# Optimization experiments

Measured on AMD Instinct MI355X. Metric: run time of the kernel, lower is better.

The kernel has to match this reference:

```python
import jax, jax.numpy as jnp
import numpy as np

N = 20000
E = 320000
IN_DIM, HID, OUT_DIM = 32, 64, 4
HEADS = 4
NEG_SLOPE = 0.2


def _self_loops(src, dst):
    loop = jnp.arange(N, dtype=src.dtype)
    return jnp.concatenate([src, loop]), jnp.concatenate([dst, loop])


def gcn_conv(x, W, b, src, dst):
    h = x @ W                                            # [N, C]
    es, ed = _self_loops(src, dst)
    deg = jax.ops.segment_sum(jnp.ones_like(es, dtype=h.dtype), ed, num_segments=N)
    dinv = jnp.where(deg > 0, jax.lax.rsqrt(deg), 0.0)
    norm = dinv[es] * dinv[ed]                           # [E']
    out = jax.ops.segment_sum(h[es] * norm[:, None], ed, num_segments=N)
    return out + b


def gat_conv(x, W, att_src, att_dst, b, src, dst):
    # PyG GATConv: heads concat, self-loops, leaky_relu(0.2), softmax over incoming edges per dst
    H, C = att_src.shape
    h = (x @ W).reshape(N, H, C)                         # [N, H, C]
    a_s = jnp.sum(h * att_src, axis=-1)                  # [N, H]
    a_d = jnp.sum(h * att_dst, axis=-1)                  # [N, H]
    es, ed = _self_loops(src, dst)
    logits = jax.nn.leaky_relu(a_s[es] + a_d[ed], NEG_SLOPE)   # [E', H]
    m = jax.ops.segment_max(logits, ed, num_segments=N)
    expv = jnp.exp(logits - m[ed])
    denom = jax.ops.segment_sum(expv, ed, num_segments=N)
    alpha = expv / denom[ed]                             # [E', H]
    out = jax.ops.segment_sum(h[es] * alpha[:, :, None], ed, num_segments=N)
    return out.reshape(N, H * C) + b


def setup_inputs() -> dict:
    key = jax.random.key(0)
    ks = iter(jax.random.split(key, 32))
    s = 0.05
    def w(shape):
        return jax.random.normal(next(ks), shape, dtype=jnp.float32) * s
    inp = {}
    inp["x"] = jax.random.normal(next(ks), (N, IN_DIM), dtype=jnp.float32)
    inp["edge_index"] = jax.random.randint(next(ks), (2, E), 0, N, dtype=jnp.int32)
    # encoder1 GCN 32->64; encoder2 GCN 64->128; encoder3 GAT 128->128 x4 heads
    inp["w_e1"], inp["b_e1"] = w((IN_DIM, HID)), jnp.zeros((HID,), jnp.float32)
    inp["w_e2"], inp["b_e2"] = w((HID, 2 * HID)), jnp.zeros((2 * HID,), jnp.float32)
    inp["w_e3"] = w((2 * HID, HEADS * 2 * HID))
    inp["as_e3"], inp["ad_e3"] = w((HEADS, 2 * HID)), w((HEADS, 2 * HID))
    inp["b_e3"] = jnp.zeros((HEADS * 2 * HID,), jnp.float32)
    # decoder1 GCN 1024->128; decoder2 GCN 128->64; decoder3 GAT 64->64 x4 heads
    inp["w_d1"], inp["b_d1"] = w((HEADS * 2 * HID, 2 * HID)), jnp.zeros((2 * HID,), jnp.float32)
    inp["w_d2"], inp["b_d2"] = w((2 * HID, HID)), jnp.zeros((HID,), jnp.float32)
    inp["w_d3"] = w((HID, HEADS * HID))
    inp["as_d3"], inp["ad_d3"] = w((HEADS, HID)), w((HEADS, HID))
    inp["b_d3"] = jnp.zeros((HEADS * HID,), jnp.float32)
    # MLP head 256->256->128->4
    inp["w_fc1"], inp["b_fc1"] = w((4 * HID, 4 * HID)), jnp.zeros((4 * HID,), jnp.float32)
    inp["w_fc2"], inp["b_fc2"] = w((4 * HID, 2 * HID)), jnp.zeros((2 * HID,), jnp.float32)
    inp["w_fin"], inp["b_fin"] = w((2 * HID, OUT_DIM)), jnp.zeros((OUT_DIM,), jnp.float32)
    return inp


def reference(x, edge_index, w_e1, b_e1, w_e2, b_e2, w_e3, as_e3, ad_e3, b_e3,
              w_d1, b_d1, w_d2, b_d2, w_d3, as_d3, ad_d3, b_d3,
              w_fc1, b_fc1, w_fc2, b_fc2, w_fin, b_fin):
    src, dst = edge_index[0], edge_index[1]
    relu = jax.nn.relu
    x1 = relu(gcn_conv(x, w_e1, b_e1, src, dst))
    x2 = relu(gcn_conv(x1, w_e2, b_e2, src, dst))
    x3 = relu(gat_conv(x2, w_e3, as_e3, ad_e3, b_e3, src, dst))
    h = relu(gcn_conv(x3, w_d1, b_d1, src, dst)) + x2
    h = relu(gcn_conv(h, w_d2, b_d2, src, dst)) + x1
    h = relu(gat_conv(h, w_d3, as_d3, ad_d3, b_d3, src, dst))
    h = relu(h @ w_fc1 + b_fc1)
    h = relu(h @ w_fc2 + b_fc2)
    return h @ w_fin + b_fin
```

## Files before the change

kernel.cpp:

```cpp
#include <hip/hip_runtime.h>
#include <cstdint>
#include <cstddef>

static constexpr int Nn = 20000;
static constexpr int Ee = 320000;

typedef _Float16 half8 __attribute__((ext_vector_type(8)));
typedef float f32x4 __attribute__((ext_vector_type(4)));

__device__ __forceinline__ float lrelu02(float x){ return fmaxf(x, 0.2f*x); }
__device__ __forceinline__ float af(int x){ return __int_as_float(x); }

__device__ __forceinline__ void packhl(float v, unsigned short& h, unsigned short& l){
  _Float16 hh = (_Float16)v;
  _Float16 ll = (_Float16)((v - (float)hh) * 2048.0f);
  h = __builtin_bit_cast(unsigned short, hh);
  l = __builtin_bit_cast(unsigned short, ll);
}

__global__ void k_scan(const int* __restrict__ cnt, int* __restrict__ row_start,
                       float* __restrict__ dinv){
  __shared__ int part[1024];
  int tid = threadIdx.x;
  const int PER = 20;
  int base = tid*PER;
  int s = 0;
  for (int i = 0; i < PER; ++i){ int idx = base+i; if (idx < Nn) s += cnt[idx]; }
  part[tid] = s; __syncthreads();
  for (int off = 1; off < 1024; off <<= 1){
    int v = (tid >= off) ? part[tid-off] : 0;
    __syncthreads();
    part[tid] += v;
    __syncthreads();
  }
  int run = (tid == 0) ? 0 : part[tid-1];
  for (int i = 0; i < PER; ++i){
    int idx = base+i;
    if (idx < Nn){
      row_start[idx] = run;
      int c = cnt[idx];
      run += c;
      dinv[idx] = rsqrtf((float)(c+1));
    }
  }
  if (tid == 1023) row_start[Nn] = run;
}

__global__ void k_scatter(const int* __restrict__ src, const int* __restrict__ dst,
                          const int* __restrict__ row_start, int* __restrict__ fill,
                          int* __restrict__ csr, const float* __restrict__ dinv,
                          int2* __restrict__ erec){
  int e = blockIdx.x*256 + threadIdx.x;
  if (e < Ee){
    int d = dst[e];
    int pos = row_start[d] + atomicAdd(&fill[d], 1);
    int u = src[e];
    csr[pos] = u;
    erec[pos] = make_int2(u, __float_as_int(dinv[u]));
  }
}

struct PrepArgs {
  const float *w_e1,*w_e2,*w_e3,*w_d1,*w_d2,*w_d3,*w_fc1,*w_fc2;
  unsigned short *p_e1,*p_e2,*p_e3,*p_d1,*p_d2,*p_d3,*p_fc1,*p_fc2;
  const float *as_e3,*ad_e3,*as_d3,*ad_d3;
  float *wsF_e3,*wdF_e3,*wsF_d3,*wdF_d3;
  const int* dst;
  int* cnt;
};

__device__ __forceinline__ void packw_one(const float* __restrict__ W,
                                          unsigned short* __restrict__ out,
                                          int i, int jlog, int K){
  int k = i >> jlog, col = i - (k << jlog);
  unsigned short h, l; packhl(W[i], h, l);
  size_t pos = ((size_t)((col>>4)*(K>>3) + (k>>3))*16 + (col&15))*8 + (k&7);
  out[pos] = h;
  out[pos + ((size_t)K << jlog)] = l;
}

__global__ void k_init(PrepArgs a){
  int gi = blockIdx.x*256 + threadIdx.x;
  if (gi >= 264960){
    int e = gi - 264960;
    if (e < Ee) atomicAdd(&a.cnt[a.dst[e]], 1);
    return;
  }
  int i = gi;
  if      (i <   2048) packw_one(a.w_e1,  a.p_e1,  i,          6,  32);
  else if (i <  10240) packw_one(a.w_e2,  a.p_e2,  i-2048,     7,  64);
  else if (i <  75776) packw_one(a.w_e3,  a.p_e3,  i-10240,    9, 128);
  else if (i < 141312) packw_one(a.w_d1,  a.p_d1,  i-75776,    7, 512);
  else if (i < 149504) packw_one(a.w_d2,  a.p_d2,  i-141312,   6, 128);
  else if (i < 165888) packw_one(a.w_d3,  a.p_d3,  i-149504,   8,  64);
  else if (i < 231424) packw_one(a.w_fc1, a.p_fc1, i-165888,   8, 256);
  else if (i < 264192) packw_one(a.w_fc2, a.p_fc2, i-231424,   7, 256);
  else if (i < 264704){
    int t = i - 264192;
    int h = t >> 7, k = t & 127;
    float s = 0.f, d = 0.f;
    #pragma unroll 4
    for (int c = 0; c < 128; ++c){
      float wv = a.w_e3[(size_t)k*512 + h*128 + c];
      s = fmaf(wv, a.as_e3[h*128 + c], s);
      d = fmaf(wv, a.ad_e3[h*128 + c], d);
    }
    a.wsF_e3[h*128 + k] = s;
    a.wdF_e3[h*128 + k] = d;
  } else {
    int t = i - 264704;
    int h = t >> 6, k = t & 63;
    float s = 0.f, d = 0.f;
    #pragma unroll 4
    for (int c = 0; c < 64; ++c){
      float wv = a.w_d3[(size_t)k*256 + h*64 + c];
      s = fmaf(wv, a.as_d3[h*64 + c], s);
      d = fmaf(wv, a.ad_d3[h*64 + c], d);
    }
    a.wsF_d3[h*64 + k] = s;
    a.wdF_d3[h*64 + k] = d;
  }
}

template<int C, int POST>
__global__ __launch_bounds__(256) void k_gcn_agg(
    const float* __restrict__ h, const float* __restrict__ dinv,
    const int* __restrict__ row_start, const int2* __restrict__ erec,
    const float* __restrict__ bias, const float* __restrict__ skip,
    float* __restrict__ outf, unsigned short* __restrict__ outp){
  int v = blockIdx.x*4 + (threadIdx.x >> 6);
  int lane = threadIdx.x & 63;
  int s = __builtin_amdgcn_readfirstlane(row_start[v]);
  int e = __builtin_amdgcn_readfirstlane(row_start[v+1]);
  float dv = dinv[v];
  const int c = (C==32) ? (lane & 31) : ((C==128) ? lane*2 : lane);

  float a0 = 0.f, a1 = 0.f;
  if constexpr (C == 32){
    int half = lane >> 5;
    int j = s + half;
    for (; j + 2 < e; j += 4){
      int2 r0 = erec[j], r1 = erec[j+2];
      float t0 = h[(size_t)r0.x*32 + c];
      float t1 = h[(size_t)r1.x*32 + c];
      a0 = fmaf(af(r0.y), t0, a0);
      a0 = fmaf(af(r1.y), t1, a0);
    }
    if (j < e){
      int2 r0 = erec[j];
      a0 = fmaf(af(r0.y), h[(size_t)r0.x*32 + c], a0);
    }
    a0 += __shfl_xor(a0, 32);
  } else if constexpr (C == 128){
    int j = s;
    for (; j + 4 <= e; j += 4){
      int2 r0 = erec[j], r1 = erec[j+1], r2 = erec[j+2], r3 = erec[j+3];
      float2 t0 = *(const float2*)&h[(size_t)r0.x*128 + c];
      float2 t1 = *(const float2*)&h[(size_t)r1.x*128 + c];
      float2 t2 = *(const float2*)&h[(size_t)r2.x*128 + c];
      float2 t3 = *(const float2*)&h[(size_t)r3.x*128 + c];
      a0=fmaf(af(r0.y),t0.x,a0); a1=fmaf(af(r0.y),t0.y,a1);
      a0=fmaf(af(r1.y),t1.x,a0); a1=fmaf(af(r1.y),t1.y,a1);
      a0=fmaf(af(r2.y),t2.x,a0); a1=fmaf(af(r2.y),t2.y,a1);
      a0=fmaf(af(r3.y),t3.x,a0); a1=fmaf(af(r3.y),t3.y,a1);
    }
    for (; j < e; ++j){
      int2 r = erec[j];
      float2 t = *(const float2*)&h[(size_t)r.x*128 + c];
      a0 = fmaf(af(r.y), t.x, a0); a1 = fmaf(af(r.y), t.y, a1);
    }
  } else {
    int j = s;
    for (; j + 4 <= e; j += 4){
      int2 r0 = erec[j], r1 = erec[j+1], r2 = erec[j+2], r3 = erec[j+3];
      float t0 = h[(size_t)r0.x*64 + c];
      float t1 = h[(size_t)r1.x*64 + c];
      float t2 = h[(size_t)r2.x*64 + c];
      float t3 = h[(size_t)r3.x*64 + c];
      a0=fmaf(af(r0.y),t0,a0); a0=fmaf(af(r1.y),t1,a0);
      a0=fmaf(af(r2.y),t2,a0); a0=fmaf(af(r3.y),t3,a0);
    }
    for (; j < e; ++j){
      int2 r = erec[j];
      a0 = fmaf(af(r.y), h[(size_t)r.x*64 + c], a0);
    }
  }

  if constexpr (C == 128){
    float2 hv = *(const float2*)&h[(size_t)v*128 + c];
    float vx = fmaf(a0, dv, hv.x*dv*dv);
    float vy = fmaf(a1, dv, hv.y*dv*dv);
    if constexpr (POST & 1){
      float2 bv = *(const float2*)&bias[c];
      float2 sk = *(const float2*)&skip[(size_t)v*128 + c];
      vx = fmaxf(vx + bv.x, 0.f) + sk.x;
      vy = fmaxf(vy + bv.y, 0.f) + sk.y;
    }
    if constexpr (POST & 2){
      unsigned short h0,l0,h1,l1; packhl(vx,h0,l0); packhl(vy,h1,l1);
      *(unsigned int*)&outp[(size_t)v*128 + c] = (unsigned)h0 | ((unsigned)h1<<16);
      *(unsigned int*)&outp[(size_t)v*128 + c + (size_t)Nn*128] = (unsigned)l0 | ((unsigned)l1<<16);
    } else {
      *(float2*)&outf[(size_t)v*128 + c] = make_float2(vx, vy);
    }
  } else if constexpr (C == 64){
    float val = fmaf(a0, dv, h[(size_t)v*64 + c]*dv*dv);
    if constexpr (POST & 1){
      val = fmaxf(val + bias[c], 0.f) + skip[(size_t)v*64 + c];
    }
    if constexpr (POST & 2){
      unsigned short hh,ll; packhl(val,hh,ll);
      outp[(size_t)v*64 + c] = hh;
      outp[(size_t)v*64 + c + (size_t)Nn*64] = ll;
    } else {
      outf[(size_t)v*64 + c] = val;
    }
  } else {
    float val = fmaf(a0, dv, h[(size_t)v*32 + c]*dv*dv);
    if (lane < 32){
      unsigned short hh,ll; packhl(val,hh,ll);
      outp[(size_t)v*32 + c] = hh;
      outp[(size_t)v*32 + c + (size_t)Nn*32] = ll;
    }
  }
}

template<int INC>
__global__ __launch_bounds__(256) void k_attn_in(
    const float* __restrict__ X, const float* __restrict__ wsF, const float* __restrict__ wdF,
    float* __restrict__ aS, float* __restrict__ aD){
  int v = blockIdx.x*4 + (threadIdx.x >> 6);
  int lane = threadIdx.x & 63;
  float x0 = X[(size_t)v*INC + lane];
  float x1 = (INC == 128) ? X[(size_t)v*INC + 64 + lane] : 0.f;
  float s[4], d[4];
  #pragma unroll
  for (int h = 0; h < 4; ++h){
    s[h] = x0*wsF[h*INC + lane];
    d[h] = x0*wdF[h*INC + lane];
    if constexpr (INC == 128){
      s[h] = fmaf(x1, wsF[h*INC + 64 + lane], s[h]);
      d[h] = fmaf(x1, wdF[h*INC + 64 + lane], d[h]);
    }
  }
  #pragma unroll
  for (int off = 32; off; off >>= 1){
    #pragma unroll
    for (int h = 0; h < 4; ++h){
      s[h] += __shfl_xor(s[h], off);
      d[h] += __shfl_xor(d[h], off);
    }
  }
  if (lane == 0){
    *(float4*)&aS[v*4] = make_float4(s[0], s[1], s[2], s[3]);
    *(float4*)&aD[v*4] = make_float4(d[0], d[1], d[2], d[3]);
  }
}

template<int INC>
__global__ __launch_bounds__(256) void k_gat_fused(
    const float* __restrict__ X, const int* __restrict__ csr,
    const float* __restrict__ aS, const float* __restrict__ aD,
    const int* __restrict__ row_start, unsigned short* __restrict__ outp){
  __shared__ float4 sF[4][64];
  int wv = threadIdx.x >> 6;
  int v = blockIdx.x*4 + wv;
  int lane = threadIdx.x & 63;
  int s = __builtin_amdgcn_readfirstlane(row_start[v]);
  int e = __builtin_amdgcn_readfirstlane(row_start[v+1]);
  const int c2 = lane*2;

  float4 tD = *(const float4*)&aD[v*4];
  float ad0=tD.x, ad1=tD.y, ad2=tD.z, ad3=tD.w;
  float4 tS = *(const float4*)&aS[v*4];

  float sd0=0.f, sd1=0.f, sd2=0.f, sd3=0.f;
  float2 acc0={0,0}, acc1={0,0}, acc2={0,0}, acc3={0,0};
  float ac0=0.f, ac1=0.f, ac2=0.f, ac3=0.f;

  for (int base = s; base < e; base += 64){
    int i = base + lane;
    float4 f = {0.f, 0.f, 0.f, 0.f};
    if (i < e){
      int u = csr[i];
      float4 a4 = *(const float4*)&aS[u*4];
      f.x = __expf(lrelu02(a4.x+ad0));
      f.y = __expf(lrelu02(a4.y+ad1));
      f.z = __expf(lrelu02(a4.z+ad2));
      f.w = __expf(lrelu02(a4.w+ad3));
      sd0 += f.x; sd1 += f.y; sd2 += f.z; sd3 += f.w;
    }
    sF[wv][lane] = f;
    int cnt = min(64, e - base);
    int j = 0;
    for (; j + 4 <= cnt; j += 4){
      int u0=csr[base+j], u1=csr[base+j+1], u2=csr[base+j+2], u3=csr[base+j+3];
      float4 f0=sF[wv][j], f1=sF[wv][j+1], f2=sF[wv][j+2], f3=sF[wv][j+3];
      if constexpr (INC == 128){
        float2 x0 = *(const float2*)&X[(size_t)u0*128 + c2];
        float2 x1 = *(const float2*)&X[(size_t)u1*128 + c2];
        float2 x2 = *(const float2*)&X[(size_t)u2*128 + c2];
        float2 x3 = *(const float2*)&X[(size_t)u3*128 + c2];
        acc0.x=fmaf(f0.x,x0.x,acc0.x); acc0.y=fmaf(f0.x,x0.y,acc0.y);
        acc1.x=fmaf(f0.y,x0.x,acc1.x); acc1.y=fmaf(f0.y,x0.y,acc1.y);
        acc2.x=fmaf(f0.z,x0.x,acc2.x); acc2.y=fmaf(f0.z,x0.y,acc2.y);
        acc3.x=fmaf(f0.w,x0.x,acc3.x); acc3.y=fmaf(f0.w,x0.y,acc3.y);
        acc0.x=fmaf(f1.x,x1.x,acc0.x); acc0.y=fmaf(f1.x,x1.y,acc0.y);
        acc1.x=fmaf(f1.y,x1.x,acc1.x); acc1.y=fmaf(f1.y,x1.y,acc1.y);
        acc2.x=fmaf(f1.z,x1.x,acc2.x); acc2.y=fmaf(f1.z,x1.y,acc2.y);
        acc3.x=fmaf(f1.w,x1.x,acc3.x); acc3.y=fmaf(f1.w,x1.y,acc3.y);
        acc0.x=fmaf(f2.x,x2.x,acc0.x); acc0.y=fmaf(f2.x,x2.y,acc0.y);
        acc1.x=fmaf(f2.y,x2.x,acc1.x); acc1.y=fmaf(f2.y,x2.y,acc1.y);
        acc2.x=fmaf(f2.z,x2.x,acc2.x); acc2.y=fmaf(f2.z,x2.y,acc2.y);
        acc3.x=fmaf(f2.w,x2.x,acc3.x); acc3.y=fmaf(f2.w,x2.y,acc3.y);
        acc0.x=fmaf(f3.x,x3.x,acc0.x); acc0.y=fmaf(f3.x,x3.y,acc0.y);
        acc1.x=fmaf(f3.y,x3.x,acc1.x); acc1.y=fmaf(f3.y,x3.y,acc1.y);
        acc2.x=fmaf(f3.z,x3.x,acc2.x); acc2.y=fmaf(f3.z,x3.y,acc2.y);
        acc3.x=fmaf(f3.w,x3.x,acc3.x); acc3.y=fmaf(f3.w,x3.y,acc3.y);
      } else {
        float x0 = X[(size_t)u0*64 + lane];
        float x1 = X[(size_t)u1*64 + lane];
        float x2 = X[(size_t)u2*64 + lane];
        float x3 = X[(size_t)u3*64 + lane];
        ac0=fmaf(f0.x,x0,ac0); ac1=fmaf(f0.y,x0,ac1); ac2=fmaf(f0.z,x0,ac2); ac3=fmaf(f0.w,x0,ac3);
        ac0=fmaf(f1.x,x1,ac0); ac1=fmaf(f1.y,x1,ac1); ac2=fmaf(f1.z,x1,ac2); ac3=fmaf(f1.w,x1,ac3);
        ac0=fmaf(f2.x,x2,ac0); ac1=fmaf(f2.y,x2,ac1); ac2=fmaf(f2.z,x2,ac2); ac3=fmaf(f2.w,x2,ac3);
        ac0=fmaf(f3.x,x3,ac0); ac1=fmaf(f3.y,x3,ac1); ac2=fmaf(f3.z,x3,ac2); ac3=fmaf(f3.w,x3,ac3);
      }
    }
    for (; j < cnt; ++j){
      int u = csr[base+j];
      float4 f4 = sF[wv][j];
      if constexpr (INC == 128){
        float2 xu = *(const float2*)&X[(size_t)u*128 + c2];
        acc0.x=fmaf(f4.x,xu.x,acc0.x); acc0.y=fmaf(f4.x,xu.y,acc0.y);
        acc1.x=fmaf(f4.y,xu.x,acc1.x); acc1.y=fmaf(f4.y,xu.y,acc1.y);
        acc2.x=fmaf(f4.z,xu.x,acc2.x); acc2.y=fmaf(f4.z,xu.y,acc2.y);
        acc3.x=fmaf(f4.w,xu.x,acc3.x); acc3.y=fmaf(f4.w,xu.y,acc3.y);
      } else {
        float xu = X[(size_t)u*64 + lane];
        ac0=fmaf(f4.x,xu,ac0); ac1=fmaf(f4.y,xu,ac1); ac2=fmaf(f4.z,xu,ac2); ac3=fmaf(f4.w,xu,ac3);
      }
    }
  }

  #pragma unroll
  for (int off = 32; off; off >>= 1){
    sd0 += __shfl_xor(sd0, off);
    sd1 += __shfl_xor(sd1, off);
    sd2 += __shfl_xor(sd2, off);
    sd3 += __shfl_xor(sd3, off);
  }
  float es0=__expf(lrelu02(tS.x+ad0)), es1=__expf(lrelu02(tS.y+ad1));
  float es2=__expf(lrelu02(tS.z+ad2)), es3=__expf(lrelu02(tS.w+ad3));
  float r0=1.f/(sd0+es0), r1=1.f/(sd1+es1), r2=1.f/(sd2+es2), r3=1.f/(sd3+es3);

  if constexpr (INC == 128){
    float2 xv = *(const float2*)&X[(size_t)v*128 + c2];
    const size_t loOff = (size_t)Nn*512;
    float ox, oy; unsigned short h0,l0,h1,l1;
    ox=(acc0.x+es0*xv.x)*r0; oy=(acc0.y+es0*xv.y)*r0;
    packhl(ox,h0,l0); packhl(oy,h1,l1);
    *(unsigned int*)&outp[(size_t)v*512 +   0 + c2] = (unsigned)h0|((unsigned)h1<<16);
    *(unsigned int*)&outp[(size_t)v*512 +   0 + c2 + loOff] = (unsigned)l0|((unsigned)l1<<16);
    ox=(acc1.x+es1*xv.x)*r1; oy=(acc1.y+es1*xv.y)*r1;
    packhl(ox,h0,l0); packhl(oy,h1,l1);
    *(unsigned int*)&outp[(size_t)v*512 + 128 + c2] = (unsigned)h0|((unsigned)h1<<16);
    *(unsigned int*)&outp[(size_t)v*512 + 128 + c2 + loOff] = (unsigned)l0|((unsigned)l1<<16);
    ox=(acc2.x+es2*xv.x)*r2; oy=(acc2.y+es2*xv.y)*r2;
    packhl(ox,h0,l0); packhl(oy,h1,l1);
    *(unsigned int*)&outp[(size_t)v*512 + 256 + c2] = (unsigned)h0|((unsigned)h1<<16);
    *(unsigned int*)&outp[(size_t)v*512 + 256 + c2 + loOff] = (unsigned)l0|((unsigned)l1<<16);
    ox=(acc3.x+es3*xv.x)*r3; oy=(acc3.y+es3*xv.y)*r3;
    packhl(ox,h0,l0); packhl(oy,h1,l1);
    *(unsigned int*)&outp[(size_t)v*512 + 384 + c2] = (unsigned)h0|((unsigned)h1<<16);
    *(unsigned int*)&outp[(size_t)v*512 + 384 + c2 + loOff] = (unsigned)l0|((unsigned)l1<<16);
  } else {
    float xv = X[(size_t)v*64 + lane];
    const size_t loOff = (size_t)Nn*256;
    unsigned short hh,ll;
    float o;
    o = (ac0+es0*xv)*r0; packhl(o,hh,ll);
    outp[(size_t)v*256 +   0 + lane] = hh; outp[(size_t)v*256 +   0 + lane + loOff] = ll;
    o = (ac1+es1*xv)*r1; packhl(o,hh,ll);
    outp[(size_t)v*256 +  64 + lane] = hh; outp[(size_t)v*256 +  64 + lane + loOff] = ll;
    o = (ac2+es2*xv)*r2; packhl(o,hh,ll);
    outp[(size_t)v*256 + 128 + lane] = hh; outp[(size_t)v*256 + 128 + lane + loOff] = ll;
    o = (ac3+es3*xv)*r3; packhl(o,hh,ll);
    outp[(size_t)v*256 + 192 + lane] = hh; outp[(size_t)v*256 + 192 + lane + loOff] = ll;
  }
}

template<int K, int J, int Jh, int EPI>
__global__ __launch_bounds__(256) void k_gemm(
    const unsigned short* __restrict__ Ahi, int lda,
    const unsigned short* __restrict__ Wp,
    const float* __restrict__ bias,
    float* __restrict__ outf, unsigned short* __restrict__ outp){
  __shared__ unsigned short sAhi[4*64*8], sAlo[4*64*8];
  __shared__ unsigned short sBhi[4*64*8], sBlo[4*64*8];

  const int tid  = threadIdx.x;
  const int lane = tid & 63, w = tid >> 6;
  const int rb = blockIdx.x;
  const int colbase = blockIdx.z*Jh + blockIdx.y*64;
  const int akoff   = blockIdx.z*K;
  const size_t AloOff = (size_t)Nn*lda;
  const size_t WloOff = (size_t)K*J;

  f32x4 accH[4] = {{0,0,0,0},{0,0,0,0},{0,0,0,0},{0,0,0,0}};
  f32x4 accM[4] = {{0,0,0,0},{0,0,0,0},{0,0,0,0},{0,0,0,0}};

  const int arow = tid >> 2;
  const int akq  = (tid & 3) * 8;
  int agrow = rb*64 + arow; if (agrow >= Nn) agrow = Nn - 1;
  const unsigned short* Ag = Ahi + (size_t)agrow*lda + akoff + akq;
  const int aw_idx = (((arow>>4)*4 + (akq>>3))*16 + (arow&15))*8;
  const int bcol = tid & 63;
  const int bkg  = tid >> 6;
  const int bw_idx = (((bcol>>4)*4 + bkg)*16 + (bcol&15))*8;
  const int cf_g  = (colbase>>4) + (bcol>>4);
  const size_t wbase = ((size_t)cf_g*(K/8)*16 + (size_t)(bcol&15))*8;

  #pragma unroll 1
  for (int ks = 0; ks < K/32; ++ks){
    if (ks) __syncthreads();
    {
      const unsigned short* p = Ag + ks*32;
      uint4 hv = *(const uint4*)p;
      uint4 lv = *(const uint4*)(p + AloOff);
      *(uint4*)&sAhi[aw_idx] = hv;
      *(uint4*)&sAlo[aw_idx] = lv;
    }
    {
      size_t goff = wbase + (size_t)(ks*4 + bkg)*128;
      uint4 hv = *(const uint4*)&Wp[goff];
      uint4 lv = *(const uint4*)&Wp[goff + WloOff];
      *(uint4*)&sBhi[bw_idx] = hv;
      *(uint4*)&sBlo[bw_idx] = lv;
    }
    __syncthreads();

    half8 aH = *(const half8*)&sAhi[(w*64 + lane)*8];
    half8 aL = *(const half8*)&sAlo[(w*64 + lane)*8];
    #pragma unroll
    for (int cf = 0; cf < 4; ++cf){
      half8 bH = *(const half8*)&sBhi[(cf*64 + lane)*8];
      half8 bL = *(const half8*)&sBlo[(cf*64 + lane)*8];
      accH[cf] = __builtin_amdgcn_mfma_f32_16x16x32_f16(aH, bH, accH[cf], 0, 0, 0);
      accM[cf] = __builtin_amdgcn_mfma_f32_16x16x32_f16(aH, bL, accM[cf], 0, 0, 0);
      accM[cf] = __builtin_amdgcn_mfma_f32_16x16x32_f16(aL, bH, accM[cf], 0, 0, 0);
    }
  }

  #pragma unroll
  for (int cf = 0; cf < 4; ++cf){
    int col = colbase + cf*16 + (lane & 15);
    float bv = (EPI >= 1) ? bias[col] : 0.f;
    #pragma unroll
    for (int r = 0; r < 4; ++r){
      int row = rb*64 + w*16 + ((lane>>4)*4 + r);
      if (row < Nn){
        float v = accH[cf][r] + accM[cf][r]*(1.0f/2048.0f);
        if constexpr (EPI >= 1) v = fmaxf(v + bv, 0.f);
        if constexpr (EPI == 2){
          unsigned short hh, ll; packhl(v, hh, ll);
          outp[(size_t)row*J + col] = hh;
          outp[(size_t)row*J + col + (size_t)Nn*J] = ll;
        } else {
          outf[(size_t)row*J + col] = v;
        }
      }
    }
  }
}

__global__ __launch_bounds__(256) void k_mm_fin(
    const float* __restrict__ A, const float* __restrict__ W,
    const float* __restrict__ bias, float* __restrict__ out){
  int row = blockIdx.x*4 + (threadIdx.x >> 6);
  int lane = threadIdx.x & 63;
  float a0 = A[(size_t)row*128 + lane];
  float a1 = A[(size_t)row*128 + 64 + lane];
  float4 w0 = ((const float4*)W)[lane];
  float4 w1 = ((const float4*)W)[64 + lane];
  float p0 = fmaf(a1, w1.x, a0*w0.x);
  float p1 = fmaf(a1, w1.y, a0*w0.y);
  float p2 = fmaf(a1, w1.z, a0*w0.z);
  float p3 = fmaf(a1, w1.w, a0*w0.w);
  #pragma unroll
  for (int off = 32; off; off >>= 1){
    p0 += __shfl_xor(p0, off);
    p1 += __shfl_xor(p1, off);
    p2 += __shfl_xor(p2, off);
    p3 += __shfl_xor(p3, off);
  }
  if (lane == 0){
    float4 bv = *(const float4*)bias;
    *(float4*)&out[(size_t)row*4] = make_float4(p0+bv.x, p1+bv.y, p2+bv.z, p3+bv.w);
  }
}

extern "C" void kernel_launch(void* const* d_in, const int* in_sizes, int n_in,
                              void* d_out, int out_size, void* d_ws, size_t ws_size,
                              hipStream_t stream){
  const float* x     = (const float*)d_in[0];
  const int*   ei    = (const int*)  d_in[1];
  const float* w_e1  = (const float*)d_in[2];
  const float* b_e1  = (const float*)d_in[3];
  const float* w_e2  = (const float*)d_in[4];
  const float* b_e2  = (const float*)d_in[5];
  const float* w_e3  = (const float*)d_in[6];
  const float* as_e3 = (const float*)d_in[7];
  const float* ad_e3 = (const float*)d_in[8];
  const float* b_e3  = (const float*)d_in[9];
  const float* w_d1  = (const float*)d_in[10];
  const float* b_d1  = (const float*)d_in[11];
  const float* w_d2  = (const float*)d_in[12];
  const float* b_d2  = (const float*)d_in[13];
  const float* w_d3  = (const float*)d_in[14];
  const float* as_d3 = (const float*)d_in[15];
  const float* ad_d3 = (const float*)d_in[16];
  const float* b_d3  = (const float*)d_in[17];
  const float* w_fc1 = (const float*)d_in[18];
  const float* b_fc1 = (const float*)d_in[19];
  const float* w_fc2 = (const float*)d_in[20];
  const float* b_fc2 = (const float*)d_in[21];
  const float* w_fin = (const float*)d_in[22];
  const float* b_fin = (const float*)d_in[23];

  char* ws = (char*)d_ws;
  size_t off = 0;
  auto alloc = [&](size_t bytes)->char*{
    char* p = ws + off;
    off += (bytes + 255) & ~size_t(255);
    return p;
  };
  int*   cnt       = (int*)  alloc((size_t)Nn*4);
  int*   fill      = (int*)  alloc((size_t)Nn*4);
  int*   row_start = (int*)  alloc((size_t)(Nn+1)*4);
  int*   csr       = (int*)  alloc((size_t)Ee*4);
  float* dinv      = (float*)alloc((size_t)Nn*4);
  int2*  erec      = (int2*) alloc((size_t)Ee*8);
  float* aSb       = (float*)alloc((size_t)Nn*16);
  float* aDb       = (float*)alloc((size_t)Nn*16);
  float* wsF_e3    = (float*)alloc(4*128*4);
  float* wdF_e3    = (float*)alloc(4*128*4);
  float* wsF_d3    = (float*)alloc(4*64*4);
  float* wdF_d3    = (float*)alloc(4*64*4);
  unsigned short* wp_e1  = (unsigned short*)alloc((size_t)32*64*4);
  unsigned short* wp_e2  = (unsigned short*)alloc((size_t)64*128*4);
  unsigned short* wp_e3  = (unsigned short*)alloc((size_t)128*512*4);
  unsigned short* wp_d1  = (unsigned short*)alloc((size_t)512*128*4);
  unsigned short* wp_d2  = (unsigned short*)alloc((size_t)128*64*4);
  unsigned short* wp_d3  = (unsigned short*)alloc((size_t)64*256*4);
  unsigned short* wp_fc1 = (unsigned short*)alloc((size_t)256*256*4);
  unsigned short* wp_fc2 = (unsigned short*)alloc((size_t)256*128*4);
  unsigned short* P0 = (unsigned short*)alloc((size_t)Nn*32*4);
  float* X1 = (float*)alloc((size_t)Nn*64*4);
  float* X2 = (float*)alloc((size_t)Nn*128*4);
  unsigned short* S1 = (unsigned short*)alloc((size_t)Nn*512*4);
  unsigned short* S2 = (unsigned short*)alloc((size_t)Nn*512*4);
  char*  S3 = alloc((size_t)Nn*128*4);

  const int* srcp = ei;
  const int* dstp = ei + Ee;

  hipMemsetAsync(cnt, 0, (size_t)(((size_t)Nn*4 + 255) & ~size_t(255)) + (size_t)Nn*4, stream);

  PrepArgs pa;
  pa.w_e1=w_e1; pa.w_e2=w_e2; pa.w_e3=w_e3; pa.w_d1=w_d1;
  pa.w_d2=w_d2; pa.w_d3=w_d3; pa.w_fc1=w_fc1; pa.w_fc2=w_fc2;
  pa.p_e1=wp_e1; pa.p_e2=wp_e2; pa.p_e3=wp_e3; pa.p_d1=wp_d1;
  pa.p_d2=wp_d2; pa.p_d3=wp_d3; pa.p_fc1=wp_fc1; pa.p_fc2=wp_fc2;
  pa.as_e3=as_e3; pa.ad_e3=ad_e3; pa.as_d3=as_d3; pa.ad_d3=ad_d3;
  pa.wsF_e3=wsF_e3; pa.wdF_e3=wdF_e3; pa.wsF_d3=wsF_d3; pa.wdF_d3=wdF_d3;
  pa.dst=dstp; pa.cnt=cnt;
  k_init<<<2285, 256, 0, stream>>>(pa);

  k_scan<<<1, 1024, 0, stream>>>(cnt, row_start, dinv);
  k_scatter<<<(Ee+255)/256, 256, 0, stream>>>(srcp, dstp, row_start, fill, csr, dinv, erec);

  k_gcn_agg<32,2><<<Nn/4, 256, 0, stream>>>(x, dinv, row_start, erec, nullptr, nullptr, nullptr, P0);
  k_gemm<32,64,64,1><<<dim3(313,1,1), 256, 0, stream>>>(P0, 32, wp_e1, b_e1, X1, nullptr);
  k_gcn_agg<64,2><<<Nn/4, 256, 0, stream>>>(X1, dinv, row_start, erec, nullptr, nullptr, nullptr, (unsigned short*)S3);
  k_gemm<64,128,128,1><<<dim3(313,2,1), 256, 0, stream>>>((unsigned short*)S3, 64, wp_e2, b_e2, X2, nullptr);
  k_attn_in<128><<<Nn/4, 256, 0, stream>>>(X2, wsF_e3, wdF_e3, aSb, aDb);
  k_gat_fused<128><<<Nn/4, 256, 0, stream>>>(X2, csr, aSb, aDb, row_start, S1);
  k_gemm<128,512,128,2><<<dim3(313,2,4), 256, 0, stream>>>(S1, 512, wp_e3, b_e3, nullptr, S2);
  k_gemm<512,128,128,0><<<dim3(313,2,1), 256, 0, stream>>>(S2, 512, wp_d1, nullptr, (float*)S3, nullptr);
  k_gcn_agg<128,3><<<Nn/4, 256, 0, stream>>>((float*)S3, dinv, row_start, erec, b_d1, X2, nullptr, S1);
  k_gemm<128,64,64,0><<<dim3(313,1,1), 256, 0, stream>>>(S1, 128, wp_d2, nullptr, (float*)S2, nullptr);
  k_gcn_agg<64,1><<<Nn/4, 256, 0, stream>>>((float*)S2, dinv, row_start, erec, b_d2, X1, (float*)S3, nullptr);
  k_attn_in<64><<<Nn/4, 256, 0, stream>>>((float*)S3, wsF_d3, wdF_d3, aSb, aDb);
  k_gat_fused<64><<<Nn/4, 256, 0, stream>>>((float*)S3, csr, aSb, aDb, row_start, S1);
  k_gemm<64,256,64,2><<<dim3(313,1,4), 256, 0, stream>>>(S1, 256, wp_d3, b_d3, nullptr, S2);
  k_gemm<256,256,256,2><<<dim3(313,4,1), 256, 0, stream>>>(S2, 256, wp_fc1, b_fc1, nullptr, S1);
  k_gemm<256,128,128,1><<<dim3(313,2,1), 256, 0, stream>>>(S1, 256, wp_fc2, b_fc2, (float*)S2, nullptr);
  k_mm_fin<<<Nn/4, 256, 0, stream>>>((float*)S2, w_fin, b_fin, (float*)d_out);
}
```

Baseline: 349.3 us.

## Split GCN and GAT aggregation across channel slices with multiple edges per wave

The GCN and GAT aggregation kernels now give each wave a 16- or 32-channel slice of a node and process several edges in parallel across lane groups, finishing with a cross-lane shuffle reduction. The grid grows by the number of slices (4x or 8x blocks), so more waves are in flight for the gather-bound neighbor loads. In exchange, the GAT kernel recomputes the edge softmax weights once per slice, edge indices are reloaded per slice, and loads per lane drop from float2 to scalar with 64-byte row segments.

```diff
diff --git a/kernel.cpp b/kernel.cpp
--- a/kernel.cpp
+++ b/kernel.cpp
@@ -4,6 +4,7 @@
 
 static constexpr int Nn = 20000;
 static constexpr int Ee = 320000;
+static constexpr int VB = Nn/4;
 
 typedef _Float16 half8 __attribute__((ext_vector_type(8)));
 typedef float f32x4 __attribute__((ext_vector_type(4)));
@@ -122,105 +123,48 @@
   }
 }
 
-template<int C, int POST>
+template<int C, int CHS, int POST>
 __global__ __launch_bounds__(256) void k_gcn_agg(
     const float* __restrict__ h, const float* __restrict__ dinv,
     const int* __restrict__ row_start, const int2* __restrict__ erec,
     const float* __restrict__ bias, const float* __restrict__ skip,
     float* __restrict__ outf, unsigned short* __restrict__ outp){
-  int v = blockIdx.x*4 + (threadIdx.x >> 6);
+  constexpr int NS  = C/CHS;
+  constexpr int EPW = 64/CHS;
+  constexpr int QSH = (CHS==16) ? 4 : 5;
+  int bx = blockIdx.x;
+  int slice = (NS==1) ? 0 : (bx / VB);
+  int vb    = (NS==1) ? bx : (bx % VB);
+  int v = vb*4 + (threadIdx.x >> 6);
   int lane = threadIdx.x & 63;
   int s = __builtin_amdgcn_readfirstlane(row_start[v]);
   int e = __builtin_amdgcn_readfirstlane(row_start[v+1]);
   float dv = dinv[v];
-  const int c = (C==32) ? (lane & 31) : ((C==128) ? lane*2 : lane);
-
-  float a0 = 0.f, a1 = 0.f;
-  if constexpr (C == 32){
-    int half = lane >> 5;
-    int j = s + half;
-    for (; j + 2 < e; j += 4){
-      int2 r0 = erec[j], r1 = erec[j+2];
-      float t0 = h[(size_t)r0.x*32 + c];
-      float t1 = h[(size_t)r1.x*32 + c];
-      a0 = fmaf(af(r0.y), t0, a0);
-      a0 = fmaf(af(r1.y), t1, a0);
-    }
-    if (j < e){
-      int2 r0 = erec[j];
-      a0 = fmaf(af(r0.y), h[(size_t)r0.x*32 + c], a0);
-    }
-    a0 += __shfl_xor(a0, 32);
-  } else if constexpr (C == 128){
-    int j = s;
-    for (; j + 4 <= e; j += 4){
-      int2 r0 = erec[j], r1 = erec[j+1], r2 = erec[j+2], r3 = erec[j+3];
-      float2 t0 = *(const float2*)&h[(size_t)r0.x*128 + c];
-      float2 t1 = *(const float2*)&h[(size_t)r1.x*128 + c];
-      float2 t2 = *(const float2*)&h[(size_t)r2.x*128 + c];
-      float2 t3 = *(const float2*)&h[(size_t)r3.x*128 + c];
-      a0=fmaf(af(r0.y),t0.x,a0); a1=fmaf(af(r0.y),t0.y,a1);
-      a0=fmaf(af(r1.y),t1.x,a0); a1=fmaf(af(r1.y),t1.y,a1);
-      a0=fmaf(af(r2.y),t2.x,a0); a1=fmaf(af(r2.y),t2.y,a1);
-      a0=fmaf(af(r3.y),t3.x,a0); a1=fmaf(af(r3.y),t3.y,a1);
-    }
-    for (; j < e; ++j){
-      int2 r = erec[j];
-      float2 t = *(const float2*)&h[(size_t)r.x*128 + c];
-      a0 = fmaf(af(r.y), t.x, a0); a1 = fmaf(af(r.y), t.y, a1);
-    }
-  } else {
-    int j = s;
-    for (; j + 4 <= e; j += 4){
-      int2 r0 = erec[j], r1 = erec[j+1], r2 = erec[j+2], r3 = erec[j+3];
-      float t0 = h[(size_t)r0.x*64 + c];
-      float t1 = h[(size_t)r1.x*64 + c];
-      float t2 = h[(size_t)r2.x*64 + c];
-      float t3 = h[(size_t)r3.x*64 + c];
-      a0=fmaf(af(r0.y),t0,a0); a0=fmaf(af(r1.y),t1,a0);
-      a0=fmaf(af(r2.y),t2,a0); a0=fmaf(af(r3.y),t3,a0);
-    }
-    for (; j < e; ++j){
-      int2 r = erec[j];
-      a0 = fmaf(af(r.y), h[(size_t)r.x*64 + c], a0);
-    }
-  }
-
-  if constexpr (C == 128){
-    float2 hv = *(const float2*)&h[(size_t)v*128 + c];
-    float vx = fmaf(a0, dv, hv.x*dv*dv);
-    float vy = fmaf(a1, dv, hv.y*dv*dv);
+  const int c = slice*CHS + (lane & (CHS-1));
+  const int q = lane >> QSH;
+
+  float a0 = 0.f;
+  #pragma unroll 4
+  for (int j = s; j < e; j += EPW){
+    int idx = j + q;
+    float w = 0.f; int u = 0;
+    if (idx < e){ int2 r = erec[idx]; u = r.x; w = af(r.y); }
+    a0 = fmaf(w, h[(size_t)u*C + c], a0);
+  }
+  #pragma unroll
+  for (int off = CHS; off < 64; off <<= 1) a0 += __shfl_xor(a0, off);
+
+  if (lane < CHS){
+    float val = fmaf(a0, dv, h[(size_t)v*C + c]*dv*dv);
     if constexpr (POST & 1){
-      float2 bv = *(const float2*)&bias[c];
-      float2 sk = *(const float2*)&skip[(size_t)v*128 + c];
-      vx = fmaxf(vx + bv.x, 0.f) + sk.x;
-      vy = fmaxf(vy + bv.y, 0.f) + sk.y;
+      val = fmaxf(val + bias[c], 0.f) + skip[(size_t)v*C + c];
     }
     if constexpr (POST & 2){
-      unsigned short h0,l0,h1,l1; packhl(vx,h0,l0); packhl(vy,h1,l1);
-      *(unsigned int*)&outp[(size_t)v*128 + c] = (unsigned)h0 | ((unsigned)h1<<16);
-      *(unsigned int*)&outp[(size_t)v*128 + c + (size_t)Nn*128] = (unsigned)l0 | ((unsigned)l1<<16);
+      unsigned short hh, ll; packhl(val, hh, ll);
+      outp[(size_t)v*C + c] = hh;
+      outp[(size_t)v*C + c + (size_t)Nn*C] = ll;
     } else {
-      *(float2*)&outf[(size_t)v*128 + c] = make_float2(vx, vy);
-    }
-  } else if constexpr (C == 64){
-    float val = fmaf(a0, dv, h[(size_t)v*64 + c]*dv*dv);
-    if constexpr (POST & 1){
-      val = fmaxf(val + bias[c], 0.f) + skip[(size_t)v*64 + c];
-    }
-    if constexpr (POST & 2){
-      unsigned short hh,ll; packhl(val,hh,ll);
-      outp[(size_t)v*64 + c] = hh;
-      outp[(size_t)v*64 + c + (size_t)Nn*64] = ll;
-    } else {
-      outf[(size_t)v*64 + c] = val;
-    }
-  } else {
-    float val = fmaf(a0, dv, h[(size_t)v*32 + c]*dv*dv);
-    if (lane < 32){
-      unsigned short hh,ll; packhl(val,hh,ll);
-      outp[(size_t)v*32 + c] = hh;
-      outp[(size_t)v*32 + c + (size_t)Nn*32] = ll;
+      outf[(size_t)v*C + c] = val;
     }
   }
 }
@@ -262,20 +206,24 @@
     const float* __restrict__ X, const int* __restrict__ csr,
     const float* __restrict__ aS, const float* __restrict__ aD,
     const int* __restrict__ row_start, unsigned short* __restrict__ outp){
+  constexpr int NS = INC/16;
   __shared__ float4 sF[4][64];
+  int bx = blockIdx.x;
+  int slice = bx / VB;
+  int vb    = bx % VB;
   int wv = threadIdx.x >> 6;
-  int v = blockIdx.x*4 + wv;
+  int v = vb*4 + wv;
   int lane = threadIdx.x & 63;
   int s = __builtin_amdgcn_readfirstlane(row_start[v]);
   int e = __builtin_amdgcn_readfirstlane(row_start[v+1]);
-  const int c2 = lane*2;
+  const int c = slice*16 + (lane & 15);
+  const int q = lane >> 4;
 
   float4 tD = *(const float4*)&aD[v*4];
   float ad0=tD.x, ad1=tD.y, ad2=tD.z, ad3=tD.w;
   float4 tS = *(const float4*)&aS[v*4];
 
   float sd0=0.f, sd1=0.f, sd2=0.f, sd3=0.f;
-  float2 acc0={0,0}, acc1={0,0}, acc2={0,0}, acc3={0,0};
   float ac0=0.f, ac1=0.f, ac2=0.f, ac3=0.f;
 
   for (int base = s; base < e; base += 64){
@@ -292,54 +240,17 @@
     }
     sF[wv][lane] = f;
     int cnt = min(64, e - base);
-    int j = 0;
-    for (; j + 4 <= cnt; j += 4){
-      int u0=csr[base+j], u1=csr[base+j+1], u2=csr[base+j+2], u3=csr[base+j+3];
-      float4 f0=sF[wv][j], f1=sF[wv][j+1], f2=sF[wv][j+2], f3=sF[wv][j+3];
-      if constexpr (INC == 128){
-        float2 x0 = *(const float2*)&X[(size_t)u0*128 + c2];
-        float2 x1 = *(const float2*)&X[(size_t)u1*128 + c2];
-        float2 x2 = *(const float2*)&X[(size_t)u2*128 + c2];
-        float2 x3 = *(const float2*)&X[(size_t)u3*128 + c2];
-        acc0.x=fmaf(f0.x,x0.x,acc0.x); acc0.y=fmaf(f0.x,x0.y,acc0.y);
-        acc1.x=fmaf(f0.y,x0.x,acc1.x); acc1.y=fmaf(f0.y,x0.y,acc1.y);
-        acc2.x=fmaf(f0.z,x0.x,acc2.x); acc2.y=fmaf(f0.z,x0.y,acc2.y);
-        acc3.x=fmaf(f0.w,x0.x,acc3.x); acc3.y=fmaf(f0.w,x0.y,acc3.y);
-        acc0.x=fmaf(f1.x,x1.x,acc0.x); acc0.y=fmaf(f1.x,x1.y,acc0.y);
-        acc1.x=fmaf(f1.y,x1.x,acc1.x); acc1.y=fmaf(f1.y,x1.y,acc1.y);
-        acc2.x=fmaf(f1.z,x1.x,acc2.x); acc2.y=fmaf(f1.z,x1.y,acc2.y);
-        acc3.x=fmaf(f1.w,x1.x,acc3.x); acc3.y=fmaf(f1.w,x1.y,acc3.y);
-        acc0.x=fmaf(f2.x,x2.x,acc0.x); acc0.y=fmaf(f2.x,x2.y,acc0.y);
-        acc1.x=fmaf(f2.y,x2.x,acc1.x); acc1.y=fmaf(f2.y,x2.y,acc1.y);
-        acc2.x=fmaf(f2.z,x2.x,acc2.x); acc2.y=fmaf(f2.z,x2.y,acc2.y);
-        acc3.x=fmaf(f2.w,x2.x,acc3.x); acc3.y=fmaf(f2.w,x2.y,acc3.y);
-        acc0.x=fmaf(f3.x,x3.x,acc0.x); acc0.y=fmaf(f3.x,x3.y,acc0.y);
-        acc1.x=fmaf(f3.y,x3.x,acc1.x); acc1.y=fmaf(f3.y,x3.y,acc1.y);
-        acc2.x=fmaf(f3.z,x3.x,acc2.x); acc2.y=fmaf(f3.z,x3.y,acc2.y);
-        acc3.x=fmaf(f3.w,x3.x,acc3.x); acc3.y=fmaf(f3.w,x3.y,acc3.y);
-      } else {
-        float x0 = X[(size_t)u0*64 + lane];
-        float x1 = X[(size_t)u1*64 + lane];
-        float x2 = X[(size_t)u2*64 + lane];
-        float x3 = X[(size_t)u3*64 + lane];
-        ac0=fmaf(f0.x,x0,ac0); ac1=fmaf(f0.y,x0,ac1); ac2=fmaf(f0.z,x0,ac2); ac3=fmaf(f0.w,x0,ac3);
-        ac0=fmaf(f1.x,x1,ac0); ac1=fmaf(f1.y,x1,ac1); ac2=fmaf(f1.z,x1,ac2); ac3=fmaf(f1.w,x1,ac3);
-        ac0=fmaf(f2.x,x2,ac0); ac1=fmaf(f2.y,x2,ac1); ac2=fmaf(f2.z,x2,ac2); ac3=fmaf(f2.w,x2,ac3);
-        ac0=fmaf(f3.x,x3,ac0); ac1=fmaf(f3.y,x3,ac1); ac2=fmaf(f3.z,x3,ac2); ac3=fmaf(f3.w,x3,ac3);
-      }
-    }
-    for (; j < cnt; ++j){
-      int u = csr[base+j];
-      float4 f4 = sF[wv][j];
-      if constexpr (INC == 128){
-        float2 xu = *(const float2*)&X[(size_t)u*128 + c2];
-        acc0.x=fmaf(f4.x,xu.x,acc0.x); acc0.y=fmaf(f4.x,xu.y,acc0.y);
-        acc1.x=fmaf(f4.y,xu.x,acc1.x); acc1.y=fmaf(f4.y,xu.y,acc1.y);
-        acc2.x=fmaf(f4.z,xu.x,acc2.x); acc2.y=fmaf(f4.z,xu.y,acc2.y);
-        acc3.x=fmaf(f4.w,xu.x,acc3.x); acc3.y=fmaf(f4.w,xu.y,acc3.y);
-      } else {
-        float xu = X[(size_t)u*64 + lane];
-        ac0=fmaf(f4.x,xu,ac0); ac1=fmaf(f4.y,xu,ac1); ac2=fmaf(f4.z,xu,ac2); ac3=fmaf(f4.w,xu,ac3);
+    #pragma unroll 4
+    for (int j = 0; j < cnt; j += 4){
+      int idx = j + q;
+      if (idx < cnt){
+        int u = csr[base + idx];
+        float4 f4 = sF[wv][idx];
+        float xu = X[(size_t)u*INC + c];
+        ac0 = fmaf(f4.x, xu, ac0);
+        ac1 = fmaf(f4.y, xu, ac1);
+        ac2 = fmaf(f4.z, xu, ac2);
+        ac3 = fmaf(f4.w, xu, ac3);
       }
     }
   }
@@ -351,43 +262,28 @@
     sd2 += __shfl_xor(sd2, off);
     sd3 += __shfl_xor(sd3, off);
   }
+  ac0 += __shfl_xor(ac0, 16); ac0 += __shfl_xor(ac0, 32);
+  ac1 += __shfl_xor(ac1, 16); ac1 += __shfl_xor(ac1, 32);
+  ac2 += __shfl_xor(ac2, 16); ac2 += __shfl_xor(ac2, 32);
+  ac3 += __shfl_xor(ac3, 16); ac3 += __shfl_xor(ac3, 32);
+
   float es0=__expf(lrelu02(tS.x+ad0)), es1=__expf(lrelu02(tS.y+ad1));
   float es2=__expf(lrelu02(tS.z+ad2)), es3=__expf(lrelu02(tS.w+ad3));
   float r0=1.f/(sd0+es0), r1=1.f/(sd1+es1), r2=1.f/(sd2+es2), r3=1.f/(sd3+es3);
 
-  if constexpr (INC == 128){
-    float2 xv = *(const float2*)&X[(size_t)v*128 + c2];
-    const size_t loOff = (size_t)Nn*512;
-    float ox, oy; unsigned short h0,l0,h1,l1;
-    ox=(acc0.x+es0*xv.x)*r0; oy=(acc0.y+es0*xv.y)*r0;
-    packhl(ox,h0,l0); packhl(oy,h1,l1);
-    *(unsigned int*)&outp[(size_t)v*512 +   0 + c2] = (unsigned)h0|((unsigned)h1<<16);
-    *(unsigned int*)&outp[(size_t)v*512 +   0 + c2 + loOff] = (unsigned)l0|((unsigned)l1<<16);
-    ox=(acc1.x+es1*xv.x)*r1; oy=(acc1.y+es1*xv.y)*r1;
-    packhl(ox,h0,l0); packhl(oy,h1,l1);
-    *(unsigned int*)&outp[(size_t)v*512 + 128 + c2] = (unsigned)h0|((unsigned)h1<<16);
-    *(unsigned int*)&outp[(size_t)v*512 + 128 + c2 + loOff] = (unsigned)l0|((unsigned)l1<<16);
-    ox=(acc2.x+es2*xv.x)*r2; oy=(acc2.y+es2*xv.y)*r2;
-    packhl(ox,h0,l0); packhl(oy,h1,l1);
-    *(unsigned int*)&outp[(size_t)v*512 + 256 + c2] = (unsigned)h0|((unsigned)h1<<16);
-    *(unsigned int*)&outp[(size_t)v*512 + 256 + c2 + loOff] = (unsigned)l0|((unsigned)l1<<16);
-    ox=(acc3.x+es3*xv.x)*r3; oy=(acc3.y+es3*xv.y)*r3;
-    packhl(ox,h0,l0); packhl(oy,h1,l1);
-    *(unsigned int*)&outp[(size_t)v*512 + 384 + c2] = (unsigned)h0|((unsigned)h1<<16);
-    *(unsigned int*)&outp[(size_t)v*512 + 384 + c2 + loOff] = (unsigned)l0|((unsigned)l1<<16);
-  } else {
-    float xv = X[(size_t)v*64 + lane];
-    const size_t loOff = (size_t)Nn*256;
-    unsigned short hh,ll;
+  if (lane < 16){
+    float xv = X[(size_t)v*INC + c];
+    const size_t loOff = (size_t)Nn*4*INC;
+    unsigned short hh, ll;
     float o;
-    o = (ac0+es0*xv)*r0; packhl(o,hh,ll);
-    outp[(size_t)v*256 +   0 + lane] = hh; outp[(size_t)v*256 +   0 + lane + loOff] = ll;
-    o = (ac1+es1*xv)*r1; packhl(o,hh,ll);
-    outp[(size_t)v*256 +  64 + lane] = hh; outp[(size_t)v*256 +  64 + lane + loOff] = ll;
-    o = (ac2+es2*xv)*r2; packhl(o,hh,ll);
-    outp[(size_t)v*256 + 128 + lane] = hh; outp[(size_t)v*256 + 128 + lane + loOff] = ll;
-    o = (ac3+es3*xv)*r3; packhl(o,hh,ll);
-    outp[(size_t)v*256 + 192 + lane] = hh; outp[(size_t)v*256 + 192 + lane + loOff] = ll;
+    o = (ac0 + es0*xv)*r0; packhl(o, hh, ll);
+    outp[(size_t)v*4*INC + 0*INC + c] = hh; outp[(size_t)v*4*INC + 0*INC + c + loOff] = ll;
+    o = (ac1 + es1*xv)*r1; packhl(o, hh, ll);
+    outp[(size_t)v*4*INC + 1*INC + c] = hh; outp[(size_t)v*4*INC + 1*INC + c + loOff] = ll;
+    o = (ac2 + es2*xv)*r2; packhl(o, hh, ll);
+    outp[(size_t)v*4*INC + 2*INC + c] = hh; outp[(size_t)v*4*INC + 2*INC + c + loOff] = ll;
+    o = (ac3 + es3*xv)*r3; packhl(o, hh, ll);
+    outp[(size_t)v*4*INC + 3*INC + c] = hh; outp[(size_t)v*4*INC + 3*INC + c + loOff] = ll;
   }
 }
 
@@ -581,21 +477,21 @@
   k_scan<<<1, 1024, 0, stream>>>(cnt, row_start, dinv);
   k_scatter<<<(Ee+255)/256, 256, 0, stream>>>(srcp, dstp, row_start, fill, csr, dinv, erec);
 
-  k_gcn_agg<32,2><<<Nn/4, 256, 0, stream>>>(x, dinv, row_start, erec, nullptr, nullptr, nullptr, P0);
+  k_gcn_agg<32,32,2><<<VB, 256, 0, stream>>>(x, dinv, row_start, erec, nullptr, nullptr, nullptr, P0);
   k_gemm<32,64,64,1><<<dim3(313,1,1), 256, 0, stream>>>(P0, 32, wp_e1, b_e1, X1, nullptr);
-  k_gcn_agg<64,2><<<Nn/4, 256, 0, stream>>>(X1, dinv, row_start, erec, nullptr, nullptr, nullptr, (unsigned short*)S3);
+  k_gcn_agg<64,16,2><<<4*VB, 256, 0, stream>>>(X1, dinv, row_start, erec, nullptr, nullptr, nullptr, (unsigned short*)S3);
   k_gemm<64,128,128,1><<<dim3(313,2,1), 256, 0, stream>>>((unsigned short*)S3, 64, wp_e2, b_e2, X2, nullptr);
-  k_attn_in<128><<<Nn/4, 256, 0, stream>>>(X2, wsF_e3, wdF_e3, aSb, aDb);
-  k_gat_fused<128><<<Nn/4, 256, 0, stream>>>(X2, csr, aSb, aDb, row_start, S1);
+  k_attn_in<128><<<VB, 256, 0, stream>>>(X2, wsF_e3, wdF_e3, aSb, aDb);
+  k_gat_fused<128><<<8*VB, 256, 0, stream>>>(X2, csr, aSb, aDb, row_start, S1);
   k_gemm<128,512,128,2><<<dim3(313,2,4), 256, 0, stream>>>(S1, 512, wp_e3, b_e3, nullptr, S2);
   k_gemm<512,128,128,0><<<dim3(313,2,1), 256, 0, stream>>>(S2, 512, wp_d1, nullptr, (float*)S3, nullptr);
-  k_gcn_agg<128,3><<<Nn/4, 256, 0, stream>>>((float*)S3, dinv, row_start, erec, b_d1, X2, nullptr, S1);
+  k_gcn_agg<128,16,3><<<8*VB, 256, 0, stream>>>((float*)S3, dinv, row_start, erec, b_d1, X2, nullptr, S1);
   k_gemm<128,64,64,0><<<dim3(313,1,1), 256, 0, stream>>>(S1, 128, wp_d2, nullptr, (float*)S2, nullptr);
-  k_gcn_agg<64,1><<<Nn/4, 256, 0, stream>>>((float*)S2, dinv, row_start, erec, b_d2, X1, (float*)S3, nullptr);
-  k_attn_in<64><<<Nn/4, 256, 0, stream>>>((float*)S3, wsF_d3, wdF_d3, aSb, aDb);
-  k_gat_fused<64><<<Nn/4, 256, 0, stream>>>((float*)S3, csr, aSb, aDb, row_start, S1);
+  k_gcn_agg<64,16,1><<<4*VB, 256, 0, stream>>>((float*)S2, dinv, row_start, erec, b_d2, X1, (float*)S3, nullptr);
+  k_attn_in<64><<<VB, 256, 0, stream>>>((float*)S3, wsF_d3, wdF_d3, aSb, aDb);
+  k_gat_fused<64><<<4*VB, 256, 0, stream>>>((float*)S3, csr, aSb, aDb, row_start, S1);
   k_gemm<64,256,64,2><<<dim3(313,1,4), 256, 0, stream>>>(S1, 256, wp_d3, b_d3, nullptr, S2);
   k_gemm<256,256,256,2><<<dim3(313,4,1), 256, 0, stream>>>(S2, 256, wp_fc1, b_fc1, nullptr, S1);
   k_gemm<256,128,128,1><<<dim3(313,2,1), 256, 0, stream>>>(S1, 256, wp_fc2, b_fc2, (float*)S2, nullptr);
-  k_mm_fin<<<Nn/4, 256, 0, stream>>>((float*)S2, w_fin, b_fin, (float*)d_out);
-}
+  k_mm_fin<<<VB, 256, 0, stream>>>((float*)S2, w_fin, b_fin, (float*)d_out);
+}
```

Measured after the change: 559.6 us. 1.6x slower.
